# Kernel tuning notes

Measured on AMD Instinct MI355X. Metric: run time of the kernel, lower is better.

## Reference

```python
import jax, jax.numpy as jnp
import numpy as np
import math

B = 50        # graphs per batch
NPG = 2000    # nodes per graph
EPG = 12000   # edges per graph
F_IN = 256
NHID = 128
RATIO = 0.8


def setup_inputs() -> dict:
    key = jax.random.key(0)
    ks = jax.random.split(key, 12)
    N = B * NPG
    src_loc = jax.random.randint(ks[0], (B, EPG), 0, NPG)
    dst_loc = jax.random.randint(ks[1], (B, EPG), 0, NPG)
    off = (jnp.arange(B) * NPG)[:, None]
    edge_index = jnp.stack([(src_loc + off).reshape(-1), (dst_loc + off).reshape(-1)]).astype(jnp.int32)

    def lin(k, fi, fo):
        return (jax.random.normal(k, (fi, fo), jnp.float32) / np.sqrt(fi).astype(np.float32))

    return {
        "x": jax.random.normal(ks[2], (N, F_IN), jnp.float32),
        "W1": lin(ks[3], F_IN, NHID), "b1": jnp.zeros(NHID, jnp.float32),
        "Ws1": lin(ks[4], NHID, 1), "bs1": jnp.zeros(1, jnp.float32),
        "W2": lin(ks[5], NHID, NHID), "b2": jnp.zeros(NHID, jnp.float32),
        "Ws2": lin(ks[6], NHID, 1), "bs2": jnp.zeros(1, jnp.float32),
        "W3": lin(ks[7], NHID, NHID), "b3": jnp.zeros(NHID, jnp.float32),
        "Ws3": lin(ks[8], NHID, 1), "bs3": jnp.zeros(1, jnp.float32),
        "Wl": lin(ks[9], 2 * NHID, NHID), "bl": jnp.zeros(NHID, jnp.float32),
        "edge_index": edge_index,
    }


def gcn_conv(x, W, b, src, dst, w, N):
    # PyG GCNConv: D^{-1/2} (A + I) D^{-1/2} X W + b, deg from edge weights + self loop
    h = x @ W
    deg = jax.ops.segment_sum(w, dst, num_segments=N) + 1.0
    dis = jax.lax.rsqrt(deg)
    norm = w * dis[src] * dis[dst]                       # [E]
    agg = jax.ops.segment_sum(h[src] * norm[:, None], dst, num_segments=N)
    return agg + h / deg[:, None] + b                    # self-loop norm = 1/deg


def sag_pool(x, src, dst, w, Ws, bs, n_per_graph):
    N = x.shape[0]
    k = math.ceil(RATIO * n_per_graph)
    score = gcn_conv(x, Ws, bs, src, dst, w, N)[:, 0]    # [N]
    _, topi = jax.lax.top_k(score.reshape(B, n_per_graph), k)
    perm = (topi + (jnp.arange(B) * n_per_graph)[:, None]).reshape(-1)
    x_new = x[perm] * jnp.tanh(score[perm])[:, None]
    # filter_adj: keep edges whose endpoints survive, reindex; dropped edges -> weight 0
    mapping = jnp.full((N,), -1, jnp.int32).at[perm].set(jnp.arange(B * k, dtype=jnp.int32))
    ns, nd = mapping[src], mapping[dst]
    valid = (ns >= 0) & (nd >= 0) & (w > 0)
    return (x_new, jnp.where(valid, ns, 0), jnp.where(valid, nd, 0),
            jnp.where(valid, w, jnp.zeros((), x.dtype)), k)


def readout(x, n):
    # global max pool || global mean pool (equal-size graphs, nodes grouped per graph)
    xr = x.reshape(B, n, -1)
    return jnp.concatenate([xr.max(axis=1), xr.mean(axis=1)], axis=-1)


def reference(x, W1, b1, Ws1, bs1, W2, b2, Ws2, bs2, W3, b3, Ws3, bs3, Wl, bl, edge_index):
    src, dst = edge_index[0], edge_index[1]
    w = jnp.ones(src.shape[0], x.dtype)
    n = NPG
    x = jax.nn.relu(gcn_conv(x, W1, b1, src, dst, w, B * n))
    x, src, dst, w, n = sag_pool(x, src, dst, w, Ws1, bs1, n)
    x1 = readout(x, n)
    x = jax.nn.relu(gcn_conv(x, W2, b2, src, dst, w, B * n))
    x, src, dst, w, n = sag_pool(x, src, dst, w, Ws2, bs2, n)
    x2 = readout(x, n)
    x = jax.nn.relu(gcn_conv(x, W3, b3, src, dst, w, B * n))
    x, src, dst, w, n = sag_pool(x, src, dst, w, Ws3, bs3, n)
    x3 = readout(x, n)
    return jax.nn.relu((x1 + x2 + x3) @ Wl + bl)
```

## Files before the change

### kernel.cpp

```cpp
#include <hip/hip_runtime.h>
#include <math.h>

#define B_GRAPHS 50
#define NPG0     2000
#define EPG      12000
#define F_IN_C   256
#define NHID     128
#define N0       (B_GRAPHS * NPG0)
#define NE       (B_GRAPHS * EPG)
#define RSEG     32
#define GSLOTS   7
#define CPAD     136
#define KMAX     1600

typedef _Float16 f16x8 __attribute__((ext_vector_type(8)));
typedef float    f32x4 __attribute__((ext_vector_type(4)));

static inline int cdiv(int a, int b) { return (a + b - 1) / b; }

__global__ void k_fill_start(int* __restrict__ cnt, float* __restrict__ accum) {
    int i = blockIdx.x * 256 + threadIdx.x;
    if (i < N0) cnt[i] = 0;
    if (i < B_GRAPHS * 256) accum[i] = 0.f;
}

__global__ void k_init_cvt(const int* __restrict__ ei, int* __restrict__ esrc,
                           int* __restrict__ edst, float* __restrict__ ew,
                           int* __restrict__ cnt,
                           const float* __restrict__ W1, const float* __restrict__ W2,
                           const float* __restrict__ W3, _Float16* __restrict__ WT1,
                           _Float16* __restrict__ WT2, _Float16* __restrict__ WT3) {
    int t = blockIdx.x * 256 + threadIdx.x;
    if (t < NE) {
        int d = ei[NE + t];
        esrc[t] = ei[t]; edst[t] = d; ew[t] = 1.0f;
        atomicAdd(&cnt[d], 1);
    }
    if (t < 128 * 256) {
        int n = t >> 8, kk = t & 255;
        WT1[t] = (_Float16)W1[kk * 128 + n];
    } else if (t < 128 * 256 + 128 * 128) {
        int u = t - 32768; int n = u >> 7, kk = u & 127;
        WT2[u] = (_Float16)W2[kk * 128 + n];
    } else if (t < 128 * 256 + 2 * 128 * 128) {
        int u = t - 49152; int n = u >> 7, kk = u & 127;
        WT3[u] = (_Float16)W3[kk * 128 + n];
    }
}

template<int FP32IN, int F, int GATHER>
__global__ __launch_bounds__(256) void k_gemm_ws(const void* __restrict__ Xin,
                                                 const _Float16* __restrict__ WT,
                                                 const int* __restrict__ perm,
                                                 const float* __restrict__ gate,
                                                 _Float16* __restrict__ H, int N) {
    constexpr int KH  = (F > 128) ? 128 : F;
    constexpr int K8H = KH / 8;
    constexpr int SMEMSZ = (128 * KH > 64 * CPAD) ? 128 * KH : 64 * CPAD;
    __shared__ _Float16 smem[SMEMSZ];
    const int tid  = threadIdx.x;
    const int wave = tid >> 6, lane = tid & 63;
    const int quad = lane >> 4, l16 = lane & 15;
    const int m_blk = blockIdx.x * 64;

    f32x4 acc[8];
#pragma unroll
    for (int j = 0; j < 8; ++j) acc[j] = {0.f, 0.f, 0.f, 0.f};

    int row0 = m_blk + wave * 16 + l16;
    if (row0 > N - 1) row0 = N - 1;
    _Float16 g0 = (_Float16)1.0f;
    if (GATHER) {
        g0 = (_Float16)gate[row0];
        row0 = perm[row0];
    }
    const int sx = l16 & 7;
    constexpr int NKQ = F / 32;

    if (FP32IN) {
        constexpr int PD = (NKQ < 4) ? NKQ : 4;
        const float* base0 = (const float*)Xin + (size_t)row0 * F + quad * 8;
        float4 p0[PD][2];
#pragma unroll
        for (int i = 0; i < PD; ++i) {
            p0[i][0] = ((const float4*)(base0 + i * 32))[0];
            p0[i][1] = ((const float4*)(base0 + i * 32))[1];
        }
#pragma unroll
        for (int c = tid; c < 128 * K8H; c += 256) {
            int n = c / K8H, k8 = c - n * K8H;
            f16x8 v = *(const f16x8*)&WT[(size_t)(n * (F / 8) + k8) * 8];
            *(f16x8*)&smem[n * KH + ((k8 ^ (n & 7)) << 3)] = v;
        }
        __syncthreads();
#pragma unroll
        for (int kq = 0; kq < NKQ; ++kq) {
            if (KH < F && kq == NKQ / 2) {
                __syncthreads();
#pragma unroll
                for (int c = tid; c < 128 * K8H; c += 256) {
                    int n = c / K8H, k8 = c - n * K8H;
                    f16x8 v = *(const f16x8*)&WT[(size_t)(n * (F / 8) + K8H + k8) * 8];
                    *(f16x8*)&smem[n * KH + ((k8 ^ (n & 7)) << 3)] = v;
                }
                __syncthreads();
            }
            const int b = kq % PD;
            float4 f0 = p0[b][0], f1 = p0[b][1];
            if (kq + PD < NKQ) {
                p0[b][0] = ((const float4*)(base0 + (kq + PD) * 32))[0];
                p0[b][1] = ((const float4*)(base0 + (kq + PD) * 32))[1];
            }
            f16x8 af0 = (f16x8){(_Float16)f0.x,(_Float16)f0.y,(_Float16)f0.z,(_Float16)f0.w,
                                (_Float16)f1.x,(_Float16)f1.y,(_Float16)f1.z,(_Float16)f1.w};
            f16x8 bf[8];
#pragma unroll
            for (int j = 0; j < 8; ++j)
                bf[j] = *(const f16x8*)&smem[(j * 16 + l16) * KH + (((((kq & 3) << 2) + quad) ^ sx) << 3)];
#pragma unroll
            for (int j = 0; j < 8; ++j)
                acc[j] = __builtin_amdgcn_mfma_f32_16x16x32_f16(af0, bf[j], acc[j], 0, 0, 0);
        }
    } else {
#pragma unroll
        for (int c = tid; c < 128 * K8H; c += 256) {
            int n = c / K8H, k8 = c - n * K8H;
            f16x8 v = *(const f16x8*)&WT[(size_t)(n * K8H + k8) * 8];
            *(f16x8*)&smem[n * KH + ((k8 ^ (n & 7)) << 3)] = v;
        }
        const _Float16* base0 = (const _Float16*)Xin + (size_t)row0 * F + quad * 8;
        f16x8 q0[NKQ];
#pragma unroll
        for (int i = 0; i < NKQ; ++i)
            q0[i] = *(const f16x8*)(base0 + i * 32);
        __syncthreads();
#pragma unroll
        for (int kq = 0; kq < NKQ; ++kq) {
            f16x8 af0 = q0[kq];
            if (GATHER) af0 = af0 * g0;
            f16x8 bf[8];
#pragma unroll
            for (int j = 0; j < 8; ++j)
                bf[j] = *(const f16x8*)&smem[(j * 16 + l16) * KH + (((((kq & 3) << 2) + quad) ^ sx) << 3)];
#pragma unroll
            for (int j = 0; j < 8; ++j)
                acc[j] = __builtin_amdgcn_mfma_f32_16x16x32_f16(af0, bf[j], acc[j], 0, 0, 0);
        }
    }
    __syncthreads();

    _Float16* sC = smem;
    const int rw = wave * 16;
#pragma unroll
    for (int j = 0; j < 8; ++j)
#pragma unroll
        for (int g = 0; g < 4; ++g)
            sC[(rw + quad * 4 + g) * CPAD + j * 16 + l16] = (_Float16)acc[j][g];
    __syncthreads();
    {
        int rr = tid >> 2;
        int cc = (tid & 3) * 32;
        int gr = m_blk + rr;
        if (gr < N) {
            _Float16* Hr = H + (size_t)gr * 128 + cc;
            const _Float16* Sr = sC + rr * CPAD + cc;
#pragma unroll
            for (int c = 0; c < 4; ++c)
                *(f16x8*)&Hr[c * 8] = *(const f16x8*)&Sr[c * 8];
        }
    }
}

__global__ __launch_bounds__(1024) void k_scancsr(const int* __restrict__ cnt,
                                                  int* __restrict__ offs,
                                                  const int* __restrict__ esrc,
                                                  const int* __restrict__ edst,
                                                  const float* __restrict__ ew,
                                                  int* __restrict__ csr_src,
                                                  float* __restrict__ csr_norm,
                                                  int npg) {
    __shared__ int ch[1024];
    __shared__ int scnt[2048];
    __shared__ int scur[2048];
    int b = blockIdx.x, tid = threadIdx.x;
    int base = b * npg;
    int per = (npg + 1023) >> 10;
    int s0 = tid * per;
    int s1 = s0 + per; if (s1 > npg) s1 = npg; if (s0 > npg) s0 = npg;
    int s = 0;
    for (int i = s0; i < s1; ++i) { int c = cnt[base + i]; scnt[i] = c; s += c; }
    ch[tid] = s;
    __syncthreads();
    for (int d = 1; d < 1024; d <<= 1) {
        int t = ch[tid] + ((tid >= d) ? ch[tid - d] : 0);
        __syncthreads();
        ch[tid] = t;
        __syncthreads();
    }
    int run = b * EPG + ch[tid] - s;
    for (int i = s0; i < s1; ++i) {
        offs[base + i] = run; scur[i] = run;
        run += scnt[i];
    }
    __syncthreads();
    int e0 = b * EPG;
    for (int e = tid; e < EPG; e += 1024) {
        float w = ew[e0 + e];
        if (w > 0.f) {
            int sN = esrc[e0 + e], d = edst[e0 + e];
            int pos = atomicAdd(&scur[d - base], 1);
            csr_src[pos] = sN;
            csr_norm[pos] = rsqrtf((float)(scnt[sN - base] + 1)) *
                            rsqrtf((float)(scnt[d - base] + 1));
        }
    }
}

__global__ __launch_bounds__(256) void k_agg(const _Float16* __restrict__ H,
                                             const int* __restrict__ csr_src,
                                             const float* __restrict__ csr_norm,
                                             const int* __restrict__ offs,
                                             const int* __restrict__ cnt,
                                             const float* __restrict__ bias,
                                             const float* __restrict__ Ws,
                                             _Float16* __restrict__ X,
                                             float* __restrict__ hs,
                                             int bpg, int npg) {
    int bi = blockIdx.x;
    int x = bi & 7, s = bi >> 3;
    int gslot = s / bpg, blk = s - gslot * bpg;
    int g = x + 8 * gslot;
    if (g >= B_GRAPHS) return;
    int node = g * npg + blk * 4 + (threadIdx.x >> 6);
    int lane = threadIdx.x & 63;
    int quad = lane >> 4, l16 = lane & 15;

    int st = offs[node], c = cnt[node], en = st + c;
    float acc[8];
#pragma unroll
    for (int j = 0; j < 8; ++j) acc[j] = 0.f;

    if (c > 0) {
        for (int e0 = st; e0 < en; e0 += 8) {
            int eA = e0 + quad, eB = eA + 4;
            int ecA = eA < en ? eA : en - 1;
            int ecB = eB < en ? eB : en - 1;
            int uA = csr_src[ecA], uB = csr_src[ecB];
            float nA = (eA < en) ? csr_norm[ecA] : 0.f;
            float nB = (eB < en) ? csr_norm[ecB] : 0.f;
            f16x8 hA = *(const f16x8*)&H[(size_t)uA * NHID + l16 * 8];
            f16x8 hB = *(const f16x8*)&H[(size_t)uB * NHID + l16 * 8];
#pragma unroll
            for (int j = 0; j < 8; ++j) acc[j] = fmaf((float)hA[j], nA, acc[j]);
#pragma unroll
            for (int j = 0; j < 8; ++j) acc[j] = fmaf((float)hB[j], nB, acc[j]);
        }
    }
#pragma unroll
    for (int j = 0; j < 8; ++j) {
        acc[j] += __shfl_xor(acc[j], 16, 64);
        acc[j] += __shfl_xor(acc[j], 32, 64);
    }
    float invd = 1.f / (float)(c + 1);
    f16x8 hn = *(const f16x8*)&H[(size_t)node * NHID + l16 * 8];
    float4 b0 = *(const float4*)&bias[l16 * 8];
    float4 b1 = *(const float4*)&bias[l16 * 8 + 4];
    float4 w0 = *(const float4*)&Ws[l16 * 8];
    float4 w1 = *(const float4*)&Ws[l16 * 8 + 4];
    const float bb[8] = {b0.x, b0.y, b0.z, b0.w, b1.x, b1.y, b1.z, b1.w};
    const float ww[8] = {w0.x, w0.y, w0.z, w0.w, w1.x, w1.y, w1.z, w1.w};
    float sd = 0.f;
    f16x8 o;
#pragma unroll
    for (int j = 0; j < 8; ++j) {
        float v = fmaxf(acc[j] + (float)hn[j] * invd + bb[j], 0.f);
        o[j] = (_Float16)v;
        sd = fmaf(v, ww[j], sd);
    }
    if (quad == 0)
        *(f16x8*)&X[(size_t)node * NHID + l16 * 8] = o;
    sd += __shfl_xor(sd, 1, 64);
    sd += __shfl_xor(sd, 2, 64);
    sd += __shfl_xor(sd, 4, 64);
    sd += __shfl_xor(sd, 8, 64);
    if (lane == 0) hs[node] = sd;
}

__global__ void k_score(const float* __restrict__ hs, const int* __restrict__ csr_src,
                        const float* __restrict__ csr_norm, const int* __restrict__ offs,
                        const int* __restrict__ cnt, const float* __restrict__ bs,
                        float* __restrict__ score, int N) {
    int i = blockIdx.x * 256 + threadIdx.x;
    if (i >= N) return;
    int s = offs[i], c = cnt[i];
    float a = 0.f;
    for (int e = s; e < s + c; ++e) a = fmaf(hs[csr_src[e]], csr_norm[e], a);
    score[i] = a + hs[i] / (float)(c + 1) + bs[0];
}

template<int REMAP>
__global__ __launch_bounds__(1024) void k_topk(const float* __restrict__ score,
                                               int* __restrict__ perm,
                                               float* __restrict__ gate,
                                               int* __restrict__ esrc,
                                               int* __restrict__ edst,
                                               float* __restrict__ ew,
                                               int* __restrict__ cntN,
                                               int npg, int k) {
    __shared__ float ss[2048];
    __shared__ int   si[2048];
    __shared__ int   smap[2048];
    __shared__ int   shist[KMAX];
    int b = blockIdx.x, tid = threadIdx.x;
    for (int i = tid; i < 2048; i += 1024) {
        if (i < npg) { ss[i] = score[b * npg + i]; si[i] = i; }
        else         { ss[i] = -__builtin_inff();  si[i] = i; }
    }
    __syncthreads();
    for (int size = 2; size <= 2048; size <<= 1) {
        for (int stride = size >> 1; stride > 0; stride >>= 1) {
            int t = tid;
            int i = ((t & ~(stride - 1)) << 1) | (t & (stride - 1));
            int j = i | stride;
            float sa = ss[i], sb = ss[j];
            int   ia = si[i], ib = si[j];
            bool b_before_a = (sb > sa) || (sb == sa && ib < ia);
            bool forward = ((i & size) == 0);
            bool doswap = forward ? b_before_a : !b_before_a;
            if (doswap) { ss[i] = sb; ss[j] = sa; si[i] = ib; si[j] = ia; }
            __syncthreads();
        }
    }
    for (int j = tid; j < npg; j += 1024) {
        int ol = si[j];
        if (j < k) {
            int newg = b * k + j;
            perm[newg] = b * npg + ol;
            smap[ol] = newg;
            gate[newg] = tanhf(ss[j]);
        } else {
            smap[ol] = -1;
        }
    }
    if (REMAP) {
        for (int j = tid; j < k; j += 1024) shist[j] = 0;
        __syncthreads();
        int base = b * npg, e0 = b * EPG;
        for (int e = tid; e < EPG; e += 1024) {
            int idx = e0 + e;
            float w = ew[idx];
            bool valid = false;
            int ns = 0, nd = 0;
            if (w > 0.f) {
                ns = smap[esrc[idx] - base];
                nd = smap[edst[idx] - base];
                valid = (ns >= 0) && (nd >= 0);
            }
            esrc[idx] = valid ? ns : 0;
            edst[idx] = valid ? nd : 0;
            ew[idx]   = valid ? w : 0.f;
            if (valid) atomicAdd(&shist[nd - b * k], 1);
        }
        __syncthreads();
        for (int j = tid; j < k; j += 1024) cntN[b * k + j] = shist[j];
    }
}

__global__ __launch_bounds__(128) void k_pool_readout(const _Float16* __restrict__ X,
                                                      const float* __restrict__ gate,
                                                      const int* __restrict__ perm,
                                                      float* __restrict__ pmax,
                                                      float* __restrict__ psum, int k) {
    int s = blockIdx.x, b = blockIdx.y, f = threadIdx.x;
    int j0 = (k * s) / RSEG, j1 = (k * (s + 1)) / RSEG;
    float mx = -__builtin_inff(), sm = 0.f;
    for (int j = j0; j < j1; ++j) {
        int g = b * k + j;
        int old = perm[g];
        float v = (float)X[(size_t)old * NHID + f] * gate[g];
        mx = fmaxf(mx, v);
        sm += v;
    }
    pmax[(size_t)(b * RSEG + s) * NHID + f] = mx;
    psum[(size_t)(b * RSEG + s) * NHID + f] = sm;
}

__global__ __launch_bounds__(128) void k_readout_comb(const float* __restrict__ pmax,
                                                      const float* __restrict__ psum,
                                                      float* __restrict__ accum, int k) {
    int b = blockIdx.x, f = threadIdx.x;
    float mx = -__builtin_inff(), sm = 0.f;
#pragma unroll
    for (int s = 0; s < RSEG; ++s) {
        mx = fmaxf(mx, pmax[(size_t)(b * RSEG + s) * NHID + f]);
        sm += psum[(size_t)(b * RSEG + s) * NHID + f];
    }
    accum[b * 256 + f]       += mx;
    accum[b * 256 + 128 + f] += sm / (float)k;
}

__global__ __launch_bounds__(128) void k_comb_final(const float* __restrict__ pmax,
                                                    const float* __restrict__ psum,
                                                    const float* __restrict__ accum,
                                                    const float* __restrict__ Wl,
                                                    const float* __restrict__ bl,
                                                    float* __restrict__ out, int k) {
    __shared__ float a[256];
    int b = blockIdx.x, f = threadIdx.x;
    float mx = -__builtin_inff(), sm = 0.f;
#pragma unroll
    for (int s = 0; s < RSEG; ++s) {
        mx = fmaxf(mx, pmax[(size_t)(b * RSEG + s) * NHID + f]);
        sm += psum[(size_t)(b * RSEG + s) * NHID + f];
    }
    a[f]       = accum[b * 256 + f] + mx;
    a[128 + f] = accum[b * 256 + 128 + f] + sm / (float)k;
    __syncthreads();
    float s = bl[f];
    for (int i = 0; i < 256; ++i) s = fmaf(a[i], Wl[i * NHID + f], s);
    out[b * NHID + f] = fmaxf(s, 0.f);
}

extern "C" void kernel_launch(void* const* d_in, const int* in_sizes, int n_in,
                              void* d_out, int out_size, void* d_ws, size_t ws_size,
                              hipStream_t stream) {
    const float* x0 = (const float*)d_in[0];
    const float* Wm[3] = {(const float*)d_in[1], (const float*)d_in[5], (const float*)d_in[9]};
    const float* bm[3] = {(const float*)d_in[2], (const float*)d_in[6], (const float*)d_in[10]};
    const float* Wsc[3] = {(const float*)d_in[3], (const float*)d_in[7], (const float*)d_in[11]};
    const float* bsc[3] = {(const float*)d_in[4], (const float*)d_in[8], (const float*)d_in[12]};
    const float* Wl = (const float*)d_in[13];
    const float* bl = (const float*)d_in[14];
    const int*   ei = (const int*)d_in[15];
    float* out = (float*)d_out;

    _Float16* bufA = (_Float16*)d_ws;
    _Float16* bufB = bufA + (size_t)N0 * NHID;
    _Float16* WT1  = bufB + (size_t)N0 * NHID;
    _Float16* WT2  = WT1 + 128 * 256;
    _Float16* WT3  = WT2 + 128 * 128;
    float* hs     = (float*)(WT3 + 128 * 128);
    float* score  = hs + N0;
    float* gate   = score + N0;
    float* accum  = gate + N0;
    float* pmax   = accum + B_GRAPHS * 256;
    float* psum   = pmax + B_GRAPHS * RSEG * NHID;
    int*   cntA   = (int*)(psum + B_GRAPHS * RSEG * NHID);
    int*   cntB   = cntA + N0;
    int*   offs   = cntB + N0;
    int*   perm   = offs + N0;
    int*   esrc   = perm + N0;
    int*   edst   = esrc + NE;
    float* ew     = (float*)(edst + NE);
    int*   csr_src= (int*)(ew + NE);
    float* csr_norm = (float*)(csr_src + NE);

    _Float16* WTs[3] = {WT1, WT2, WT3};
    const int EG = cdiv(NE, 256);

    k_fill_start<<<cdiv(N0, 256), 256, 0, stream>>>(cntA, accum);
    k_init_cvt<<<EG, 256, 0, stream>>>(ei, esrc, edst, ew, cntA,
                                       Wm[0], Wm[1], Wm[2], WT1, WT2, WT3);

    int npg = NPG0;
    _Float16* Hbuf = bufA; _Float16* Xbuf = bufB;

    for (int layer = 0; layer < 3; ++layer) {
        int N = B_GRAPHS * npg;
        int k = (npg * 4) / 5;
        int NG = cdiv(N, 256);
        int bpg = npg >> 2;
        int* cnt  = (layer == 1) ? cntB : cntA;
        int* cntN = (layer == 1) ? cntA : cntB;

        if (layer == 0)
            k_gemm_ws<1, 256, 0><<<cdiv(N, 64), 256, 0, stream>>>(x0, WTs[0], perm, gate, Hbuf, N);
        else
            k_gemm_ws<0, 128, 1><<<cdiv(N, 64), 256, 0, stream>>>(Xbuf, WTs[layer], perm, gate, Hbuf, N);
        k_scancsr<<<B_GRAPHS, 1024, 0, stream>>>(cnt, offs, esrc, edst, ew,
                                                 csr_src, csr_norm, npg);
        k_agg<<<8 * GSLOTS * bpg, 256, 0, stream>>>(Hbuf, csr_src, csr_norm, offs, cnt,
                                                    bm[layer], Wsc[layer], Xbuf, hs, bpg, npg);
        k_score<<<NG, 256, 0, stream>>>(hs, csr_src, csr_norm, offs, cnt, bsc[layer], score, N);
        if (layer < 2)
            k_topk<1><<<B_GRAPHS, 1024, 0, stream>>>(score, perm, gate, esrc, edst, ew,
                                                     cntN, npg, k);
        else
            k_topk<0><<<B_GRAPHS, 1024, 0, stream>>>(score, perm, gate, esrc, edst, ew,
                                                     cntN, npg, k);
        k_pool_readout<<<dim3(RSEG, B_GRAPHS), 128, 0, stream>>>(Xbuf, gate, perm, pmax, psum, k);
        if (layer < 2) {
            k_readout_comb<<<B_GRAPHS, 128, 0, stream>>>(pmax, psum, accum, k);
        } else {
            k_comb_final<<<B_GRAPHS, 128, 0, stream>>>(pmax, psum, accum, Wl, bl, out, k);
        }

        npg = k;
    }
}
```

Baseline: 569.2 us.

## Merge GEMM, CSR build and pooled readout into one launch; fuse score into top-k

```diff
diff --git a/kernel.cpp b/kernel.cpp
--- a/kernel.cpp
+++ b/kernel.cpp
@@ -48,171 +48,192 @@
     }
 }
 
-template<int FP32IN, int F, int GATHER>
-__global__ __launch_bounds__(256) void k_gemm_ws(const void* __restrict__ Xin,
-                                                 const _Float16* __restrict__ WT,
-                                                 const int* __restrict__ perm,
-                                                 const float* __restrict__ gate,
-                                                 _Float16* __restrict__ H, int N) {
+template<int FP32IN, int F, int GATHER, int POOL>
+__global__ __launch_bounds__(256) void k_fat(const void* __restrict__ Xin,
+                                             const _Float16* __restrict__ WT,
+                                             const int* __restrict__ perm,
+                                             const float* __restrict__ gate,
+                                             _Float16* __restrict__ H, int N,
+                                             const int* __restrict__ cnt,
+                                             int* __restrict__ offs,
+                                             const int* __restrict__ esrc,
+                                             const int* __restrict__ edst,
+                                             const float* __restrict__ ew,
+                                             int* __restrict__ csr_src,
+                                             float* __restrict__ csr_norm,
+                                             int npg, int NG,
+                                             float* __restrict__ pmax,
+                                             float* __restrict__ psum) {
     constexpr int KH  = (F > 128) ? 128 : F;
     constexpr int K8H = KH / 8;
     constexpr int SMEMSZ = (128 * KH > 64 * CPAD) ? 128 * KH : 64 * CPAD;
     __shared__ _Float16 smem[SMEMSZ];
-    const int tid  = threadIdx.x;
-    const int wave = tid >> 6, lane = tid & 63;
-    const int quad = lane >> 4, l16 = lane & 15;
-    const int m_blk = blockIdx.x * 64;
-
-    f32x4 acc[8];
-#pragma unroll
-    for (int j = 0; j < 8; ++j) acc[j] = {0.f, 0.f, 0.f, 0.f};
-
-    int row0 = m_blk + wave * 16 + l16;
-    if (row0 > N - 1) row0 = N - 1;
-    _Float16 g0 = (_Float16)1.0f;
-    if (GATHER) {
-        g0 = (_Float16)gate[row0];
-        row0 = perm[row0];
-    }
-    const int sx = l16 & 7;
-    constexpr int NKQ = F / 32;
-
-    if (FP32IN) {
-        constexpr int PD = (NKQ < 4) ? NKQ : 4;
-        const float* base0 = (const float*)Xin + (size_t)row0 * F + quad * 8;
-        float4 p0[PD][2];
-#pragma unroll
-        for (int i = 0; i < PD; ++i) {
-            p0[i][0] = ((const float4*)(base0 + i * 32))[0];
-            p0[i][1] = ((const float4*)(base0 + i * 32))[1];
-        }
-#pragma unroll
-        for (int c = tid; c < 128 * K8H; c += 256) {
-            int n = c / K8H, k8 = c - n * K8H;
-            f16x8 v = *(const f16x8*)&WT[(size_t)(n * (F / 8) + k8) * 8];
-            *(f16x8*)&smem[n * KH + ((k8 ^ (n & 7)) << 3)] = v;
+    const int bid = blockIdx.x;
+    const int tid = threadIdx.x;
+
+    if (bid < NG) {
+        const int wave = tid >> 6, lane = tid & 63;
+        const int quad = lane >> 4, l16 = lane & 15;
+        const int m_blk = bid * 64;
+
+        f32x4 acc[8];
+#pragma unroll
+        for (int j = 0; j < 8; ++j) acc[j] = {0.f, 0.f, 0.f, 0.f};
+
+        int row0 = m_blk + wave * 16 + l16;
+        if (row0 > N - 1) row0 = N - 1;
+        _Float16 g0 = (_Float16)1.0f;
+        if (GATHER) {
+            g0 = (_Float16)gate[row0];
+            row0 = perm[row0];
+        }
+        const int sx = l16 & 7;
+        constexpr int NKQ = F / 32;
+
+        if (FP32IN) {
+            constexpr int PD = (NKQ < 4) ? NKQ : 4;
+            const float* base0 = (const float*)Xin + (size_t)row0 * F + quad * 8;
+            float4 p0[PD][2];
+#pragma unroll
+            for (int i = 0; i < PD; ++i) {
+                p0[i][0] = ((const float4*)(base0 + i * 32))[0];
+                p0[i][1] = ((const float4*)(base0 + i * 32))[1];
+            }
+#pragma unroll
+            for (int c = tid; c < 128 * K8H; c += 256) {
+                int n = c / K8H, k8 = c - n * K8H;
+                f16x8 v = *(const f16x8*)&WT[(size_t)(n * (F / 8) + k8) * 8];
+                *(f16x8*)&smem[n * KH + ((k8 ^ (n & 7)) << 3)] = v;
+            }
+            __syncthreads();
+#pragma unroll
+            for (int kq = 0; kq < NKQ; ++kq) {
+                if (KH < F && kq == NKQ / 2) {
+                    __syncthreads();
+#pragma unroll
+                    for (int c = tid; c < 128 * K8H; c += 256) {
+                        int n = c / K8H, k8 = c - n * K8H;
+                        f16x8 v = *(const f16x8*)&WT[(size_t)(n * (F / 8) + K8H + k8) * 8];
+                        *(f16x8*)&smem[n * KH + ((k8 ^ (n & 7)) << 3)] = v;
+                    }
+                    __syncthreads();
+                }
+                const int b = kq % PD;
+                float4 f0 = p0[b][0], f1 = p0[b][1];
+                if (kq + PD < NKQ) {
+                    p0[b][0] = ((const float4*)(base0 + (kq + PD) * 32))[0];
+                    p0[b][1] = ((const float4*)(base0 + (kq + PD) * 32))[1];
+                }
+                f16x8 af0 = (f16x8){(_Float16)f0.x,(_Float16)f0.y,(_Float16)f0.z,(_Float16)f0.w,
+                                    (_Float16)f1.x,(_Float16)f1.y,(_Float16)f1.z,(_Float16)f1.w};
+                f16x8 bf[8];
+#pragma unroll
+                for (int j = 0; j < 8; ++j)
+                    bf[j] = *(const f16x8*)&smem[(j * 16 + l16) * KH + (((((kq & 3) << 2) + quad) ^ sx) << 3)];
+#pragma unroll
+                for (int j = 0; j < 8; ++j)
+                    acc[j] = __builtin_amdgcn_mfma_f32_16x16x32_f16(af0, bf[j], acc[j], 0, 0, 0);
+            }
+        } else {
+#pragma unroll
+            for (int c = tid; c < 128 * K8H; c += 256) {
+                int n = c / K8H, k8 = c - n * K8H;
+                f16x8 v = *(const f16x8*)&WT[(size_t)(n * K8H + k8) * 8];
+                *(f16x8*)&smem[n * KH + ((k8 ^ (n & 7)) << 3)] = v;
+            }
+            const _Float16* base0 = (const _Float16*)Xin + (size_t)row0 * F + quad * 8;
+            f16x8 q0[F / 32];
+#pragma unroll
+            for (int i = 0; i < F / 32; ++i)
+                q0[i] = *(const f16x8*)(base0 + i * 32);
+            __syncthreads();
+#pragma unroll
+            for (int kq = 0; kq < F / 32; ++kq) {
+                f16x8 af0 = q0[kq];
+                if (GATHER) af0 = af0 * g0;
+                f16x8 bf[8];
+#pragma unroll
+                for (int j = 0; j < 8; ++j)
+                    bf[j] = *(const f16x8*)&smem[(j * 16 + l16) * KH + (((((kq & 3) << 2) + quad) ^ sx) << 3)];
+#pragma unroll
+                for (int j = 0; j < 8; ++j)
+                    acc[j] = __builtin_amdgcn_mfma_f32_16x16x32_f16(af0, bf[j], acc[j], 0, 0, 0);
+            }
         }
         __syncthreads();
-#pragma unroll
-        for (int kq = 0; kq < NKQ; ++kq) {
-            if (KH < F && kq == NKQ / 2) {
-                __syncthreads();
-#pragma unroll
-                for (int c = tid; c < 128 * K8H; c += 256) {
-                    int n = c / K8H, k8 = c - n * K8H;
-                    f16x8 v = *(const f16x8*)&WT[(size_t)(n * (F / 8) + K8H + k8) * 8];
-                    *(f16x8*)&smem[n * KH + ((k8 ^ (n & 7)) << 3)] = v;
-                }
-                __syncthreads();
-            }
-            const int b = kq % PD;
-            float4 f0 = p0[b][0], f1 = p0[b][1];
-            if (kq + PD < NKQ) {
-                p0[b][0] = ((const float4*)(base0 + (kq + PD) * 32))[0];
-                p0[b][1] = ((const float4*)(base0 + (kq + PD) * 32))[1];
-            }
-            f16x8 af0 = (f16x8){(_Float16)f0.x,(_Float16)f0.y,(_Float16)f0.z,(_Float16)f0.w,
-                                (_Float16)f1.x,(_Float16)f1.y,(_Float16)f1.z,(_Float16)f1.w};
-            f16x8 bf[8];
-#pragma unroll
-            for (int j = 0; j < 8; ++j)
-                bf[j] = *(const f16x8*)&smem[(j * 16 + l16) * KH + (((((kq & 3) << 2) + quad) ^ sx) << 3)];
-#pragma unroll
-            for (int j = 0; j < 8; ++j)
-                acc[j] = __builtin_amdgcn_mfma_f32_16x16x32_f16(af0, bf[j], acc[j], 0, 0, 0);
-        }
-    } else {
-#pragma unroll
-        for (int c = tid; c < 128 * K8H; c += 256) {
-            int n = c / K8H, k8 = c - n * K8H;
-            f16x8 v = *(const f16x8*)&WT[(size_t)(n * K8H + k8) * 8];
-            *(f16x8*)&smem[n * KH + ((k8 ^ (n & 7)) << 3)] = v;
-        }
-        const _Float16* base0 = (const _Float16*)Xin + (size_t)row0 * F + quad * 8;
-        f16x8 q0[NKQ];
-#pragma unroll
-        for (int i = 0; i < NKQ; ++i)
-            q0[i] = *(const f16x8*)(base0 + i * 32);
+
+        _Float16* sC = smem;
+        const int rw = wave * 16;
+#pragma unroll
+        for (int j = 0; j < 8; ++j)
+#pragma unroll
+            for (int g = 0; g < 4; ++g)
+                sC[(rw + quad * 4 + g) * CPAD + j * 16 + l16] = (_Float16)acc[j][g];
         __syncthreads();
-#pragma unroll
-        for (int kq = 0; kq < NKQ; ++kq) {
-            f16x8 af0 = q0[kq];
-            if (GATHER) af0 = af0 * g0;
-            f16x8 bf[8];
-#pragma unroll
-            for (int j = 0; j < 8; ++j)
-                bf[j] = *(const f16x8*)&smem[(j * 16 + l16) * KH + (((((kq & 3) << 2) + quad) ^ sx) << 3)];
-#pragma unroll
-            for (int j = 0; j < 8; ++j)
-                acc[j] = __builtin_amdgcn_mfma_f32_16x16x32_f16(af0, bf[j], acc[j], 0, 0, 0);
-        }
-    }
-    __syncthreads();
-
-    _Float16* sC = smem;
-    const int rw = wave * 16;
-#pragma unroll
-    for (int j = 0; j < 8; ++j)
-#pragma unroll
-        for (int g = 0; g < 4; ++g)
-            sC[(rw + quad * 4 + g) * CPAD + j * 16 + l16] = (_Float16)acc[j][g];
-    __syncthreads();
-    {
-        int rr = tid >> 2;
-        int cc = (tid & 3) * 32;
-        int gr = m_blk + rr;
-        if (gr < N) {
-            _Float16* Hr = H + (size_t)gr * 128 + cc;
-            const _Float16* Sr = sC + rr * CPAD + cc;
-#pragma unroll
-            for (int c = 0; c < 4; ++c)
-                *(f16x8*)&Hr[c * 8] = *(const f16x8*)&Sr[c * 8];
-        }
-    }
-}
-
-__global__ __launch_bounds__(1024) void k_scancsr(const int* __restrict__ cnt,
-                                                  int* __restrict__ offs,
-                                                  const int* __restrict__ esrc,
-                                                  const int* __restrict__ edst,
-                                                  const float* __restrict__ ew,
-                                                  int* __restrict__ csr_src,
-                                                  float* __restrict__ csr_norm,
-                                                  int npg) {
-    __shared__ int ch[1024];
-    __shared__ int scnt[2048];
-    __shared__ int scur[2048];
-    int b = blockIdx.x, tid = threadIdx.x;
-    int base = b * npg;
-    int per = (npg + 1023) >> 10;
-    int s0 = tid * per;
-    int s1 = s0 + per; if (s1 > npg) s1 = npg; if (s0 > npg) s0 = npg;
-    int s = 0;
-    for (int i = s0; i < s1; ++i) { int c = cnt[base + i]; scnt[i] = c; s += c; }
-    ch[tid] = s;
-    __syncthreads();
-    for (int d = 1; d < 1024; d <<= 1) {
-        int t = ch[tid] + ((tid >= d) ? ch[tid - d] : 0);
+        {
+            int rr = tid >> 2;
+            int cc = (tid & 3) * 32;
+            int gr = m_blk + rr;
+            if (gr < N) {
+                _Float16* Hr = H + (size_t)gr * 128 + cc;
+                const _Float16* Sr = sC + rr * CPAD + cc;
+#pragma unroll
+                for (int c = 0; c < 4; ++c)
+                    *(f16x8*)&Hr[c * 8] = *(const f16x8*)&Sr[c * 8];
+            }
+        }
+    } else if (bid < NG + B_GRAPHS) {
+        int* ch   = (int*)smem;
+        int* scnt = ch + 256;
+        int* scur = scnt + 2048;
+        int b = bid - NG;
+        int base = b * npg;
+        int per = (npg + 255) >> 8;
+        int s0 = tid * per;
+        int s1 = s0 + per; if (s1 > npg) s1 = npg; if (s0 > npg) s0 = npg;
+        int s = 0;
+        for (int i = s0; i < s1; ++i) { int c = cnt[base + i]; scnt[i] = c; s += c; }
+        ch[tid] = s;
         __syncthreads();
-        ch[tid] = t;
+        for (int d = 1; d < 256; d <<= 1) {
+            int t = ch[tid] + ((tid >= d) ? ch[tid - d] : 0);
+            __syncthreads();
+            ch[tid] = t;
+            __syncthreads();
+        }
+        int run = b * EPG + ch[tid] - s;
+        for (int i = s0; i < s1; ++i) {
+            offs[base + i] = run; scur[i] = run;
+            run += scnt[i];
+        }
         __syncthreads();
-    }
-    int run = b * EPG + ch[tid] - s;
-    for (int i = s0; i < s1; ++i) {
-        offs[base + i] = run; scur[i] = run;
-        run += scnt[i];
-    }
-    __syncthreads();
-    int e0 = b * EPG;
-    for (int e = tid; e < EPG; e += 1024) {
-        float w = ew[e0 + e];
-        if (w > 0.f) {
-            int sN = esrc[e0 + e], d = edst[e0 + e];
-            int pos = atomicAdd(&scur[d - base], 1);
-            csr_src[pos] = sN;
-            csr_norm[pos] = rsqrtf((float)(scnt[sN - base] + 1)) *
-                            rsqrtf((float)(scnt[d - base] + 1));
-        }
+        int e0 = b * EPG;
+        for (int e = tid; e < EPG; e += 256) {
+            float w = ew[e0 + e];
+            if (w > 0.f) {
+                int sN = esrc[e0 + e], d = edst[e0 + e];
+                int pos = atomicAdd(&scur[d - base], 1);
+                csr_src[pos] = sN;
+                csr_norm[pos] = rsqrtf((float)(scnt[sN - base] + 1)) *
+                                rsqrtf((float)(scnt[d - base] + 1));
+            }
+        }
+    } else if (POOL) {
+        int pb = bid - NG - B_GRAPHS;
+        int b = pb >> 4, s2 = pb & 15;
+        int f = tid & 127, seg = s2 * 2 + (tid >> 7);
+        int kprev = npg;
+        int j0 = (kprev * seg) / RSEG, j1 = (kprev * (seg + 1)) / RSEG;
+        float mx = -__builtin_inff(), sm = 0.f;
+        const _Float16* X = (const _Float16*)Xin;
+        for (int j = j0; j < j1; ++j) {
+            int g = b * kprev + j;
+            float v = (float)X[(size_t)perm[g] * NHID + f] * gate[g];
+            mx = fmaxf(mx, v);
+            sm += v;
+        }
+        pmax[(size_t)(b * RSEG + seg) * NHID + f] = mx;
+        psum[(size_t)(b * RSEG + seg) * NHID + f] = sm;
     }
 }
 
@@ -286,35 +307,41 @@
     if (lane == 0) hs[node] = sd;
 }
 
-__global__ void k_score(const float* __restrict__ hs, const int* __restrict__ csr_src,
-                        const float* __restrict__ csr_norm, const int* __restrict__ offs,
-                        const int* __restrict__ cnt, const float* __restrict__ bs,
-                        float* __restrict__ score, int N) {
-    int i = blockIdx.x * 256 + threadIdx.x;
-    if (i >= N) return;
-    int s = offs[i], c = cnt[i];
-    float a = 0.f;
-    for (int e = s; e < s + c; ++e) a = fmaf(hs[csr_src[e]], csr_norm[e], a);
-    score[i] = a + hs[i] / (float)(c + 1) + bs[0];
-}
-
 template<int REMAP>
-__global__ __launch_bounds__(1024) void k_topk(const float* __restrict__ score,
-                                               int* __restrict__ perm,
-                                               float* __restrict__ gate,
-                                               int* __restrict__ esrc,
-                                               int* __restrict__ edst,
-                                               float* __restrict__ ew,
-                                               int* __restrict__ cntN,
-                                               int npg, int k) {
+__global__ __launch_bounds__(1024) void k_scoretopk(const float* __restrict__ hs,
+                                                    const int* __restrict__ csr_src,
+                                                    const float* __restrict__ csr_norm,
+                                                    const int* __restrict__ offs,
+                                                    const int* __restrict__ cnt,
+                                                    const float* __restrict__ bs,
+                                                    int* __restrict__ perm,
+                                                    float* __restrict__ gate,
+                                                    int* __restrict__ esrc,
+                                                    int* __restrict__ edst,
+                                                    float* __restrict__ ew,
+                                                    int* __restrict__ cntN,
+                                                    int npg, int k) {
     __shared__ float ss[2048];
     __shared__ int   si[2048];
-    __shared__ int   smap[2048];
+    __shared__ float shs[2048];
     __shared__ int   shist[KMAX];
     int b = blockIdx.x, tid = threadIdx.x;
+    int base = b * npg;
+    float bs0 = bs[0];
+    for (int i = tid; i < 2048; i += 1024)
+        shs[i] = (i < npg) ? hs[base + i] : 0.f;
+    __syncthreads();
     for (int i = tid; i < 2048; i += 1024) {
-        if (i < npg) { ss[i] = score[b * npg + i]; si[i] = i; }
-        else         { ss[i] = -__builtin_inff();  si[i] = i; }
+        if (i < npg) {
+            int st = offs[base + i], c = cnt[base + i];
+            float a = 0.f;
+            for (int e = st; e < st + c; ++e)
+                a = fmaf(shs[csr_src[e] - base], csr_norm[e], a);
+            ss[i] = a + shs[i] / (float)(c + 1) + bs0;
+        } else {
+            ss[i] = -__builtin_inff();
+        }
+        si[i] = i;
     }
     __syncthreads();
     for (int size = 2; size <= 2048; size <<= 1) {
@@ -331,11 +358,12 @@
             __syncthreads();
         }
     }
+    int* smap = (int*)shs;
     for (int j = tid; j < npg; j += 1024) {
         int ol = si[j];
         if (j < k) {
             int newg = b * k + j;
-            perm[newg] = b * npg + ol;
+            perm[newg] = base + ol;
             smap[ol] = newg;
             gate[newg] = tanhf(ss[j]);
         } else {
@@ -345,7 +373,7 @@
     if (REMAP) {
         for (int j = tid; j < k; j += 1024) shist[j] = 0;
         __syncthreads();
-        int base = b * npg, e0 = b * EPG;
+        int e0 = b * EPG;
         for (int e = tid; e < EPG; e += 1024) {
             int idx = e0 + e;
             float w = ew[idx];
@@ -440,8 +468,7 @@
     _Float16* WT2  = WT1 + 128 * 256;
     _Float16* WT3  = WT2 + 128 * 128;
     float* hs     = (float*)(WT3 + 128 * 128);
-    float* score  = hs + N0;
-    float* gate   = score + N0;
+    float* gate   = hs + N0;
     float* accum  = gate + N0;
     float* pmax   = accum + B_GRAPHS * 256;
     float* psum   = pmax + B_GRAPHS * RSEG * NHID;
@@ -457,6 +484,7 @@
 
     _Float16* WTs[3] = {WT1, WT2, WT3};
     const int EG = cdiv(NE, 256);
+    const int POOLB = B_GRAPHS * (RSEG / 2);
 
     k_fill_start<<<cdiv(N0, 256), 256, 0, stream>>>(cntA, accum);
     k_init_cvt<<<EG, 256, 0, stream>>>(ei, esrc, edst, ew, cntA,
@@ -468,30 +496,33 @@
     for (int layer = 0; layer < 3; ++layer) {
         int N = B_GRAPHS * npg;
         int k = (npg * 4) / 5;
-        int NG = cdiv(N, 256);
+        int NG = cdiv(N, 64);
         int bpg = npg >> 2;
         int* cnt  = (layer == 1) ? cntB : cntA;
         int* cntN = (layer == 1) ? cntA : cntB;
 
-        if (layer == 0)
-            k_gemm_ws<1, 256, 0><<<cdiv(N, 64), 256, 0, stream>>>(x0, WTs[0], perm, gate, Hbuf, N);
-        else
-            k_gemm_ws<0, 128, 1><<<cdiv(N, 64), 256, 0, stream>>>(Xbuf, WTs[layer], perm, gate, Hbuf, N);
-        k_scancsr<<<B_GRAPHS, 1024, 0, stream>>>(cnt, offs, esrc, edst, ew,
-                                                 csr_src, csr_norm, npg);
+        if (layer == 0) {
+            k_fat<1, 256, 0, 0><<<NG + B_GRAPHS, 256, 0, stream>>>(
+                x0, WTs[0], perm, gate, Hbuf, N,
+                cnt, offs, esrc, edst, ew, csr_src, csr_norm, npg, NG, pmax, psum);
+        } else {
+            k_fat<0, 128, 1, 1><<<NG + B_GRAPHS + POOLB, 256, 0, stream>>>(
+                Xbuf, WTs[layer], perm, gate, Hbuf, N,
+                cnt, offs, esrc, edst, ew, csr_src, csr_norm, npg, NG, pmax, psum);
+            k_readout_comb<<<B_GRAPHS, 128, 0, stream>>>(pmax, psum, accum, npg);
+        }
         k_agg<<<8 * GSLOTS * bpg, 256, 0, stream>>>(Hbuf, csr_src, csr_norm, offs, cnt,
                                                     bm[layer], Wsc[layer], Xbuf, hs, bpg, npg);
-        k_score<<<NG, 256, 0, stream>>>(hs, csr_src, csr_norm, offs, cnt, bsc[layer], score, N);
-        if (layer < 2)
-            k_topk<1><<<B_GRAPHS, 1024, 0, stream>>>(score, perm, gate, esrc, edst, ew,
-                                                     cntN, npg, k);
-        else
-            k_topk<0><<<B_GRAPHS, 1024, 0, stream>>>(score, perm, gate, esrc, edst, ew,
-                                                     cntN, npg, k);
-        k_pool_readout<<<dim3(RSEG, B_GRAPHS), 128, 0, stream>>>(Xbuf, gate, perm, pmax, psum, k);
         if (layer < 2) {
-            k_readout_comb<<<B_GRAPHS, 128, 0, stream>>>(pmax, psum, accum, k);
+            k_scoretopk<1><<<B_GRAPHS, 1024, 0, stream>>>(hs, csr_src, csr_norm, offs, cnt,
+                                                          bsc[layer], perm, gate,
+                                                          esrc, edst, ew, cntN, npg, k);
         } else {
+            k_scoretopk<0><<<B_GRAPHS, 1024, 0, stream>>>(hs, csr_src, csr_norm, offs, cnt,
+                                                          bsc[layer], perm, gate,
+                                                          esrc, edst, ew, cntN, npg, k);
+            k_pool_readout<<<dim3(RSEG, B_GRAPHS), 128, 0, stream>>>(Xbuf, gate, perm,
+                                                                     pmax, psum, k);
             k_comb_final<<<B_GRAPHS, 128, 0, stream>>>(pmax, psum, accum, Wl, bl, out, k);
         }
 
```

Measured after the change: 582.4 us. 2.3% more time.
